# Performance work log

Measured on AMD Instinct MI355X. Metric: run time of the kernel, lower is better.

The kernel has to match this reference:

```python
import jax, jax.numpy as jnp
import numpy as np

BETA = 0.25

def setup_inputs() -> dict:
    key = jax.random.key(0)
    k1, k2 = jax.random.split(key)
    z = jax.random.normal(k1, (32, 1024, 256), dtype=jnp.float32)
    codebook = jax.random.uniform(k2, (256, 8192), dtype=jnp.float32)  # (code_dim, num_codes)
    return {"z": z, "codebook": codebook}

def reference(z, codebook):
    code_dim = codebook.shape[0]
    z_flat = z.reshape(-1, code_dim)                                   # [N, D]
    # squared-distance matrix: ||z||^2 - 2 z@C + ||c||^2  -> [N, K]
    d = (jnp.sum(z_flat ** 2, axis=1, keepdims=True)
         - 2.0 * jnp.dot(z_flat, codebook)
         + jnp.sum(codebook ** 2, axis=0, keepdims=True))
    indices = jnp.argmin(d, axis=1)                                    # [N]
    z_q = codebook.T[indices].reshape(z.shape)                         # gather codes
    commitment_loss = BETA * jnp.mean((jax.lax.stop_gradient(z_q) - z) ** 2)
    codebook_loss = jnp.mean((z_q - jax.lax.stop_gradient(z)) ** 2)
    z_q_ste = z + jax.lax.stop_gradient(z_q - z)                       # straight-through
    loss = commitment_loss + codebook_loss
    return z_q_ste, indices.reshape(z.shape[:-1]), loss
```

## Files before the change

kernel.cpp:

```cpp
#include <hip/hip_runtime.h>
#include <hip/hip_bf16.h>
#include <stdint.h>


#define DEVINL __device__ __forceinline__

typedef int   intx4 __attribute__((ext_vector_type(4)));

#define NROWS   32768
#define DIMS    256
#define NCODES  8192
#define KMIN    ((int)0x80000000)

DEVINL int q8(float v, float s) {
  int q = __float2int_rn(v * s);
  return min(127, max(-127, q));
}
DEVINL unsigned pk4(float4 v, float s) {
  int a = q8(v.x, s), b = q8(v.y, s), c = q8(v.z, s), d = q8(v.w, s);
  return (unsigned)(a & 255) | ((unsigned)(b & 255) << 8) |
         ((unsigned)(c & 255) << 16) | ((unsigned)(d & 255) << 24);
}
DEVINL void gload_lds16(const void* g, void* lds) {
  __builtin_amdgcn_global_load_lds(
      (const __attribute__((address_space(1))) uint32_t*)(uintptr_t)g,
      (__attribute__((address_space(3))) uint32_t*)(uint32_t)(uintptr_t)lds,
      16, 0, 0);
}

__global__ void k_nrm(const float* __restrict__ cb, int* __restrict__ nrm) {
  __shared__ int p[256];
  int j = blockIdx.x * 32 + (threadIdx.x & 31);
  int seg = threadIdx.x >> 5;
  int s = 0;
  for (int i = 0; i < 32; ++i) {
    int q = q8(cb[(size_t)(seg * 32 + i) * NCODES + j], 127.0f);
    s += q * q;
  }
  p[threadIdx.x] = s;
  __syncthreads();
  if (threadIdx.x < 32) {
    int t = 0;
    for (int k = 0; k < 8; ++k) t += p[k * 32 + threadIdx.x];
    nrm[j] = (int)rintf((25.0f / 254.0f) * (float)t);
  }
}

__global__ void k_transpose(const float* __restrict__ cb, float* __restrict__ cbTf) {
  __shared__ float t[64][65];
  int j0 = blockIdx.x * 64, d0 = blockIdx.y * 64;
  int tx = threadIdx.x & 63, ty = threadIdx.x >> 6;
  #pragma unroll
  for (int i = 0; i < 16; ++i) {
    int dl = i * 4 + ty;
    t[dl][tx] = cb[(size_t)(d0 + dl) * NCODES + j0 + tx];
  }
  __syncthreads();
  #pragma unroll
  for (int i = 0; i < 16; ++i) {
    int jl = i * 4 + ty;
    cbTf[(size_t)(j0 + jl) * DIMS + d0 + tx] = t[tx][jl];
  }
}

__global__ void k_image(const float* __restrict__ cbTf, uint4* __restrict__ img) {
  int g = blockIdx.x * 256 + threadIdx.x;
  int step = g >> 11;
  int r = g & 2047;
  int wc = r >> 9, cf = (r >> 6) & 7, lgr = (r >> 4) & 3, l15 = r & 15;
  int tile = step >> 2, chunk = step & 3;
  int j = tile * 512 + wc * 128 + cf * 16 + l15;
  int d = chunk * 64 + lgr * 16;
  const float4* s4 = (const float4*)(cbTf + (size_t)j * DIMS + d);
  uint4 o;
  o.x = pk4(s4[0], 127.0f); o.y = pk4(s4[1], 127.0f);
  o.z = pk4(s4[2], 127.0f); o.w = pk4(s4[3], 127.0f);
  img[g] = o;
}

__global__ __launch_bounds__(512, 2)
void k_scan(const float* __restrict__ z, const int* __restrict__ nrm,
            const uint4* __restrict__ img, int2* __restrict__ cand) {
  __shared__ char smem[163840];
  char* const zb = smem;
  char* const bb = smem + 32768;
  const int* const nl = (const int*)(smem + 131072);

  const int t = threadIdx.x;
  const int lane = t & 63;
  const int wave = t >> 6;
  const int wgr = wave >> 2;
  const int wc  = wave & 3;
  const int l15 = lane & 15;
  const int lgr = lane >> 4;
  const int brow = blockIdx.x * 128;

  #pragma unroll
  for (int i = 0; i < 4; ++i) {
    int g = t + i * 512;
    int row = g >> 4, kb = g & 15;
    const float4* src = (const float4*)(z + (size_t)(brow + row) * DIMS + kb * 16);
    uint4 o;
    o.x = pk4(src[0], 25.0f); o.y = pk4(src[1], 25.0f);
    o.z = pk4(src[2], 25.0f); o.w = pk4(src[3], 25.0f);
    int addr = row * 256 + ((kb * 16) ^ ((row & 15) << 4));
    *(uint4*)(zb + addr) = o;
  }
  #pragma unroll
  for (int i = 0; i < 4; ++i) {
    int gi = t + i * 512;
    ((uint4*)(smem + 131072))[gi] = ((const uint4*)nrm)[gi];
  }
  {
    const uint4* gsrc = img + wave * 64 + lane;
    #pragma unroll
    for (int i = 0; i < 4; ++i)
      gload_lds16(gsrc + i * 512, bb + (i * 512 + wave * 64) * 16);
  }

  int k1[16], k2[16];
  #pragma unroll
  for (int i = 0; i < 16; ++i) { k1[i] = KMIN; k2[i] = KMIN; }

  __syncthreads();

  intx4 acc[4][8];
  int b_cur = 0, b_nxt = 1;

  #pragma unroll 1
  for (int s = 0; s < 64; ++s) {
    const int tile = s >> 2, chunk = s & 3;

    if (s < 63) {
      const uint4* gsrc = img + (size_t)(s + 1) * 2048 + wave * 64 + lane;
      char* dst = bb + b_nxt * 32768;
      #pragma unroll
      for (int i = 0; i < 4; ++i)
        gload_lds16(gsrc + i * 512, dst + (i * 512 + wave * 64) * 16);
      asm volatile("s_waitcnt vmcnt(4)" ::: "memory");
    } else {
      asm volatile("s_waitcnt vmcnt(0)" ::: "memory");
    }
    __builtin_amdgcn_s_barrier();

    const char* cbuf = bb + b_cur * 32768;

    if (chunk == 0) {
      #pragma unroll
      for (int cf = 0; cf < 8; ++cf) {
        int h = -nl[tile * 512 + wc * 128 + cf * 16 + l15];
        #pragma unroll
        for (int rf = 0; rf < 4; ++rf) acc[rf][cf] = intx4{h, h, h, h};
      }
    }

    intx4 a[4], b[8];
    #pragma unroll
    for (int rf = 0; rf < 4; ++rf) {
      int m = wgr * 64 + rf * 16 + l15;
      int by = (chunk * 64 + lgr * 16) ^ ((m & 15) << 4);
      a[rf] = *(const intx4*)(zb + m * 256 + by);
    }
    #pragma unroll
    for (int cf = 0; cf < 8; ++cf)
      b[cf] = *(const intx4*)(cbuf + (wc * 512 + cf * 64 + lane) * 16);

    #pragma unroll
    for (int rf = 0; rf < 4; ++rf)
      #pragma unroll
      for (int cf = 0; cf < 8; ++cf)
        acc[rf][cf] = __builtin_amdgcn_mfma_i32_16x16x64_i8(a[rf], b[cf], acc[rf][cf], 0, 0, 0);

    if (chunk == 3) {
      const int jinvb = 8191 - (tile * 512 + wc * 128 + l15);
      #pragma unroll
      for (int rf = 0; rf < 4; ++rf)
        #pragma unroll
        for (int cf = 0; cf < 8; ++cf) {
          int jinv = jinvb - cf * 16;
          #pragma unroll
          for (int r = 0; r < 4; ++r) {
            int si = rf * 4 + r;
            int k = ((acc[rf][cf][r] >> 5) << 13) + jinv;
            int t1 = max(k1[si], k);
            int t2 = min(k1[si], k);
            k1[si] = t1;
            k2[si] = max(k2[si], t2);
          }
        }
    }

    b_cur = b_nxt;
    b_nxt = (b_nxt == 2) ? 0 : b_nxt + 1;
  }

  #pragma unroll
  for (int rf = 0; rf < 4; ++rf)
    #pragma unroll
    for (int r = 0; r < 4; ++r) {
      int row = brow + wgr * 64 + rf * 16 + lgr * 4 + r;
      int si = rf * 4 + r;
      cand[(size_t)row * 64 + wc * 16 + l15] = make_int2(k1[si], k2[si]);
    }
}

__global__ __launch_bounds__(512)
void k_refine(const float* __restrict__ z, const float* __restrict__ cbTf,
              const int2* __restrict__ cand, float* __restrict__ zq,
              float* __restrict__ oidx, double* __restrict__ parts) {
  __shared__ double lsum[8];
  int lane = threadIdx.x & 63, wave = threadIdx.x >> 6;
  int row = blockIdx.x * 8 + wave;

  float4 z4 = ((const float4*)(z + (size_t)row * DIMS))[lane];
  int2 kp = cand[(size_t)row * 64 + lane];
  int ka = kp.x, kb = kp.y;

  double bd = 1e300; int bj = -1; float4 bc = {0.f, 0.f, 0.f, 0.f};
  for (int s = 0; s < 5; ++s) {
    int km = max(ka, kb);
    #pragma unroll
    for (int m = 1; m < 64; m <<= 1) km = max(km, __shfl_xor(km, m, 64));
    int j = 8191 - (km & 8191);
    if (ka == km) ka = KMIN; else if (kb == km) kb = KMIN;

    float4 c4 = ((const float4*)(cbTf + (size_t)j * DIMS))[lane];
    double dx = (double)z4.x - (double)c4.x;
    double dy = (double)z4.y - (double)c4.y;
    double dzv = (double)z4.z - (double)c4.z;
    double dw = (double)z4.w - (double)c4.w;
    double d = dx * dx + dy * dy + dzv * dzv + dw * dw;
    #pragma unroll
    for (int m = 1; m < 64; m <<= 1) d += __shfl_xor(d, m, 64);

    bool bt = (d < bd) || (d == bd && j < bj);
    if (bt) { bd = d; bj = j; bc = c4; }
  }

  ((float4*)(zq + (size_t)row * DIMS))[lane] = bc;
  if (lane == 0) oidx[row] = (float)bj;

  double lx = (double)bc.x - (double)z4.x;
  double ly = (double)bc.y - (double)z4.y;
  double lz = (double)bc.z - (double)z4.z;
  double lw = (double)bc.w - (double)z4.w;
  double l = lx * lx + ly * ly + lz * lz + lw * lw;
  #pragma unroll
  for (int m = 1; m < 64; m <<= 1) l += __shfl_xor(l, m, 64);
  if (lane == 0) lsum[wave] = l;
  __syncthreads();
  if (threadIdx.x == 0) {
    double s = 0;
    for (int i = 0; i < 8; ++i) s += lsum[i];
    parts[blockIdx.x] = s;
  }
}

__global__ void k_finish(const double* __restrict__ parts, float* __restrict__ out) {
  __shared__ double s[256];
  double a = 0;
  for (int i = threadIdx.x; i < 4096; i += 256) a += parts[i];
  s[threadIdx.x] = a;
  __syncthreads();
  for (int w = 128; w; w >>= 1) {
    if (threadIdx.x < w) s[threadIdx.x] += s[threadIdx.x + w];
    __syncthreads();
  }
  if (threadIdx.x == 0) out[0] = (float)(1.25 * s[0] / 8388608.0);
}

extern "C" void kernel_launch(void* const* d_in, const int* in_sizes, int n_in,
                              void* d_out, int out_size, void* d_ws, size_t ws_size,
                              hipStream_t stream) {
  const float* zin = (const float*)d_in[0];
  const float* cb  = (const float*)d_in[1];
  float* out = (float*)d_out;

  char* w = (char*)d_ws;
  int*    nrm   = (int*)w;
  float*  cbTf  = (float*)(w + 32768);
  char*   imgb  = w + 32768 + 8388608;
  int2*   cand  = (int2*)(w + 32768 + 8388608 + 2097152);
  double* parts = (double*)(w + 32768 + 8388608 + 2097152 + 16777216);

  float* zq_out   = out;
  float* idx_out  = out + 8388608;
  float* loss_out = out + 8388608 + 32768;

  k_nrm<<<dim3(256), dim3(256), 0, stream>>>(cb, nrm);
  k_transpose<<<dim3(128, 4), dim3(256), 0, stream>>>(cb, cbTf);
  k_image<<<dim3(512), dim3(256), 0, stream>>>(cbTf, (uint4*)imgb);
  k_scan<<<dim3(256), dim3(512), 0, stream>>>(zin, nrm, (const uint4*)imgb, cand);
  k_refine<<<dim3(4096), dim3(512), 0, stream>>>(zin, cbTf, cand, zq_out, idx_out, parts);
  k_finish<<<dim3(1), dim3(256), 0, stream>>>(parts, loss_out);
}
```

Measured before the change: 159.4 us.

## Halve scan block to 64 rows with double-buffered codebook tiles

```diff
diff --git a/kernel.cpp b/kernel.cpp
--- a/kernel.cpp
+++ b/kernel.cpp
@@ -78,26 +78,23 @@
   img[g] = o;
 }
 
-__global__ __launch_bounds__(512, 2)
+__global__ __launch_bounds__(256, 2)
 void k_scan(const float* __restrict__ z, const int* __restrict__ nrm,
             const uint4* __restrict__ img, int2* __restrict__ cand) {
-  __shared__ char smem[163840];
+  __shared__ char smem[81920];
   char* const zb = smem;
-  char* const bb = smem + 32768;
-  const int* const nl = (const int*)(smem + 131072);
+  char* const bb = smem + 16384;
 
   const int t = threadIdx.x;
   const int lane = t & 63;
   const int wave = t >> 6;
-  const int wgr = wave >> 2;
-  const int wc  = wave & 3;
   const int l15 = lane & 15;
   const int lgr = lane >> 4;
-  const int brow = blockIdx.x * 128;
+  const int brow = blockIdx.x * 64;
 
   #pragma unroll
   for (int i = 0; i < 4; ++i) {
-    int g = t + i * 512;
+    int g = t + i * 256;
     int row = g >> 4, kb = g & 15;
     const float4* src = (const float4*)(z + (size_t)(brow + row) * DIMS + kb * 16);
     uint4 o;
@@ -106,16 +103,11 @@
     int addr = row * 256 + ((kb * 16) ^ ((row & 15) << 4));
     *(uint4*)(zb + addr) = o;
   }
-  #pragma unroll
-  for (int i = 0; i < 4; ++i) {
-    int gi = t + i * 512;
-    ((uint4*)(smem + 131072))[gi] = ((const uint4*)nrm)[gi];
-  }
   {
     const uint4* gsrc = img + wave * 64 + lane;
     #pragma unroll
-    for (int i = 0; i < 4; ++i)
-      gload_lds16(gsrc + i * 512, bb + (i * 512 + wave * 64) * 16);
+    for (int i = 0; i < 8; ++i)
+      gload_lds16(gsrc + i * 256, bb + (i * 256 + wave * 64) * 16);
   }
 
   int k1[16], k2[16];
@@ -125,30 +117,29 @@
   __syncthreads();
 
   intx4 acc[4][8];
-  int b_cur = 0, b_nxt = 1;
 
   #pragma unroll 1
   for (int s = 0; s < 64; ++s) {
     const int tile = s >> 2, chunk = s & 3;
 
+    if (s > 0) {
+      asm volatile("s_waitcnt vmcnt(0)" ::: "memory");
+      __builtin_amdgcn_s_barrier();
+    }
     if (s < 63) {
       const uint4* gsrc = img + (size_t)(s + 1) * 2048 + wave * 64 + lane;
-      char* dst = bb + b_nxt * 32768;
-      #pragma unroll
-      for (int i = 0; i < 4; ++i)
-        gload_lds16(gsrc + i * 512, dst + (i * 512 + wave * 64) * 16);
-      asm volatile("s_waitcnt vmcnt(4)" ::: "memory");
-    } else {
-      asm volatile("s_waitcnt vmcnt(0)" ::: "memory");
-    }
-    __builtin_amdgcn_s_barrier();
-
-    const char* cbuf = bb + b_cur * 32768;
+      char* dst = bb + ((s + 1) & 1) * 32768;
+      #pragma unroll
+      for (int i = 0; i < 8; ++i)
+        gload_lds16(gsrc + i * 256, dst + (i * 256 + wave * 64) * 16);
+    }
+
+    const char* cbuf = bb + (s & 1) * 32768;
 
     if (chunk == 0) {
       #pragma unroll
       for (int cf = 0; cf < 8; ++cf) {
-        int h = -nl[tile * 512 + wc * 128 + cf * 16 + l15];
+        int h = -nrm[tile * 512 + wave * 128 + cf * 16 + l15];
         #pragma unroll
         for (int rf = 0; rf < 4; ++rf) acc[rf][cf] = intx4{h, h, h, h};
       }
@@ -157,13 +148,13 @@
     intx4 a[4], b[8];
     #pragma unroll
     for (int rf = 0; rf < 4; ++rf) {
-      int m = wgr * 64 + rf * 16 + l15;
-      int by = (chunk * 64 + lgr * 16) ^ ((m & 15) << 4);
+      int m = rf * 16 + l15;
+      int by = (chunk * 64 + lgr * 16) ^ (l15 << 4);
       a[rf] = *(const intx4*)(zb + m * 256 + by);
     }
     #pragma unroll
     for (int cf = 0; cf < 8; ++cf)
-      b[cf] = *(const intx4*)(cbuf + (wc * 512 + cf * 64 + lane) * 16);
+      b[cf] = *(const intx4*)(cbuf + (wave * 512 + cf * 64 + lane) * 16);
 
     #pragma unroll
     for (int rf = 0; rf < 4; ++rf)
@@ -172,7 +163,7 @@
         acc[rf][cf] = __builtin_amdgcn_mfma_i32_16x16x64_i8(a[rf], b[cf], acc[rf][cf], 0, 0, 0);
 
     if (chunk == 3) {
-      const int jinvb = 8191 - (tile * 512 + wc * 128 + l15);
+      const int jinvb = 8191 - (tile * 512 + wave * 128 + l15);
       #pragma unroll
       for (int rf = 0; rf < 4; ++rf)
         #pragma unroll
@@ -189,18 +180,15 @@
           }
         }
     }
-
-    b_cur = b_nxt;
-    b_nxt = (b_nxt == 2) ? 0 : b_nxt + 1;
   }
 
   #pragma unroll
   for (int rf = 0; rf < 4; ++rf)
     #pragma unroll
     for (int r = 0; r < 4; ++r) {
-      int row = brow + wgr * 64 + rf * 16 + lgr * 4 + r;
+      int row = brow + rf * 16 + lgr * 4 + r;
       int si = rf * 4 + r;
-      cand[(size_t)row * 64 + wc * 16 + l15] = make_int2(k1[si], k2[si]);
+      cand[(size_t)row * 64 + wave * 16 + l15] = make_int2(k1[si], k2[si]);
     }
 }
 
@@ -290,7 +278,7 @@
   k_nrm<<<dim3(256), dim3(256), 0, stream>>>(cb, nrm);
   k_transpose<<<dim3(128, 4), dim3(256), 0, stream>>>(cb, cbTf);
   k_image<<<dim3(512), dim3(256), 0, stream>>>(cbTf, (uint4*)imgb);
-  k_scan<<<dim3(256), dim3(512), 0, stream>>>(zin, nrm, (const uint4*)imgb, cand);
+  k_scan<<<dim3(512), dim3(256), 0, stream>>>(zin, nrm, (const uint4*)imgb, cand);
   k_refine<<<dim3(4096), dim3(512), 0, stream>>>(zin, cbTf, cand, zq_out, idx_out, parts);
   k_finish<<<dim3(1), dim3(256), 0, stream>>>(parts, loss_out);
 }
```

Measured after the change: 163.8 us. 2.8% more time.

## Double-buffer codebook in 64KB steps, read norms from global, use med3 for top-2

Applied to the files above, without the earlier changes.

```diff
diff --git a/kernel.cpp b/kernel.cpp
--- a/kernel.cpp
+++ b/kernel.cpp
@@ -84,7 +84,6 @@
   __shared__ char smem[163840];
   char* const zb = smem;
   char* const bb = smem + 32768;
-  const int* const nl = (const int*)(smem + 131072);
 
   const int t = threadIdx.x;
   const int lane = t & 63;
@@ -106,15 +105,10 @@
     int addr = row * 256 + ((kb * 16) ^ ((row & 15) << 4));
     *(uint4*)(zb + addr) = o;
   }
-  #pragma unroll
-  for (int i = 0; i < 4; ++i) {
-    int gi = t + i * 512;
-    ((uint4*)(smem + 131072))[gi] = ((const uint4*)nrm)[gi];
-  }
   {
     const uint4* gsrc = img + wave * 64 + lane;
     #pragma unroll
-    for (int i = 0; i < 4; ++i)
+    for (int i = 0; i < 8; ++i)
       gload_lds16(gsrc + i * 512, bb + (i * 512 + wave * 64) * 16);
   }
 
@@ -125,53 +119,56 @@
   __syncthreads();
 
   intx4 acc[4][8];
-  int b_cur = 0, b_nxt = 1;
 
   #pragma unroll 1
-  for (int s = 0; s < 64; ++s) {
-    const int tile = s >> 2, chunk = s & 3;
-
-    if (s < 63) {
-      const uint4* gsrc = img + (size_t)(s + 1) * 2048 + wave * 64 + lane;
-      char* dst = bb + b_nxt * 32768;
-      #pragma unroll
-      for (int i = 0; i < 4; ++i)
+  for (int w = 0; w < 32; ++w) {
+    const int tile = w >> 1;
+
+    if (w > 0) {
+      asm volatile("s_waitcnt vmcnt(0)" ::: "memory");
+      __builtin_amdgcn_s_barrier();
+    }
+    if (w < 31) {
+      const uint4* gsrc = img + (size_t)(w + 1) * 4096 + wave * 64 + lane;
+      char* dst = bb + ((w + 1) & 1) * 65536;
+      #pragma unroll
+      for (int i = 0; i < 8; ++i)
         gload_lds16(gsrc + i * 512, dst + (i * 512 + wave * 64) * 16);
-      asm volatile("s_waitcnt vmcnt(4)" ::: "memory");
-    } else {
-      asm volatile("s_waitcnt vmcnt(0)" ::: "memory");
-    }
-    __builtin_amdgcn_s_barrier();
-
-    const char* cbuf = bb + b_cur * 32768;
-
-    if (chunk == 0) {
+    }
+
+    const char* cbuf = bb + (w & 1) * 65536;
+
+    if ((w & 1) == 0) {
       #pragma unroll
       for (int cf = 0; cf < 8; ++cf) {
-        int h = -nl[tile * 512 + wc * 128 + cf * 16 + l15];
+        int h = -nrm[tile * 512 + wc * 128 + cf * 16 + l15];
         #pragma unroll
         for (int rf = 0; rf < 4; ++rf) acc[rf][cf] = intx4{h, h, h, h};
       }
     }
 
-    intx4 a[4], b[8];
-    #pragma unroll
-    for (int rf = 0; rf < 4; ++rf) {
-      int m = wgr * 64 + rf * 16 + l15;
-      int by = (chunk * 64 + lgr * 16) ^ ((m & 15) << 4);
-      a[rf] = *(const intx4*)(zb + m * 256 + by);
-    }
-    #pragma unroll
-    for (int cf = 0; cf < 8; ++cf)
-      b[cf] = *(const intx4*)(cbuf + (wc * 512 + cf * 64 + lane) * 16);
-
-    #pragma unroll
-    for (int rf = 0; rf < 4; ++rf)
+    #pragma unroll
+    for (int half = 0; half < 2; ++half) {
+      const int chunk = (w & 1) * 2 + half;
+      intx4 a[4], b[8];
+      #pragma unroll
+      for (int rf = 0; rf < 4; ++rf) {
+        int m = wgr * 64 + rf * 16 + l15;
+        int by = (chunk * 64 + lgr * 16) ^ ((m & 15) << 4);
+        a[rf] = *(const intx4*)(zb + m * 256 + by);
+      }
       #pragma unroll
       for (int cf = 0; cf < 8; ++cf)
-        acc[rf][cf] = __builtin_amdgcn_mfma_i32_16x16x64_i8(a[rf], b[cf], acc[rf][cf], 0, 0, 0);
-
-    if (chunk == 3) {
+        b[cf] = *(const intx4*)(cbuf + half * 32768 + (wc * 512 + cf * 64 + lane) * 16);
+
+      #pragma unroll
+      for (int rf = 0; rf < 4; ++rf)
+        #pragma unroll
+        for (int cf = 0; cf < 8; ++cf)
+          acc[rf][cf] = __builtin_amdgcn_mfma_i32_16x16x64_i8(a[rf], b[cf], acc[rf][cf], 0, 0, 0);
+    }
+
+    if (w & 1) {
       const int jinvb = 8191 - (tile * 512 + wc * 128 + l15);
       #pragma unroll
       for (int rf = 0; rf < 4; ++rf)
@@ -183,15 +180,14 @@
             int si = rf * 4 + r;
             int k = ((acc[rf][cf][r] >> 5) << 13) + jinv;
             int t1 = max(k1[si], k);
-            int t2 = min(k1[si], k);
+            int nk2;
+            asm("v_med3_i32 %0, %1, %2, %3"
+                : "=v"(nk2) : "v"(k), "v"(k1[si]), "v"(k2[si]));
+            k2[si] = nk2;
             k1[si] = t1;
-            k2[si] = max(k2[si], t2);
           }
         }
     }
-
-    b_cur = b_nxt;
-    b_nxt = (b_nxt == 2) ? 0 : b_nxt + 1;
   }
 
   #pragma unroll
```

New measurement: 162.6 us. 1.02x slower.
